# Performance work log

Hardware: AMD Instinct MI355X
Metric: run time of the kernel (lower is better)

The kernel has to match this reference:

```python
import jax, jax.numpy as jnp
import numpy as np

B = 8; C = 256; NH = 8; CH = C // NH; MLP_H = 4 * C; EPS = 1e-5
SIZES = [(56, 56), (28, 28), (14, 14), (7, 7)]  # scales 2..5; scale1 (112x112) passes through


def _layernorm(x, g, b):
    mu = jnp.mean(x, -1, keepdims=True)
    var = jnp.mean((x - mu) ** 2, -1, keepdims=True)
    return (x - mu) * jax.lax.rsqrt(var + EPS) * g + b


def _dwconv(x, w, b, pad):
    # x: [B, C, H, W], w: [C, 1, k, k] depthwise
    out = jax.lax.conv_general_dilated(
        x, w, (1, 1), [(pad, pad), (pad, pad)],
        feature_group_count=x.shape[1],
        dimension_numbers=('NCHW', 'OIHW', 'NCHW'))
    return out + b[None, :, None, None]


def _cpe(x, w, b, size):
    # ConvPosEnc: depthwise 3x3 conv residual on image tokens, cls untouched
    Hh, Ww = size
    Bb, N, Cc = x.shape
    cls_tok, img = x[:, :1], x[:, 1:]
    feat = img.transpose(0, 2, 1).reshape(Bb, Cc, Hh, Ww)
    feat = _dwconv(feat, w, b, 1) + feat
    img = feat.reshape(Bb, Cc, Hh * Ww).transpose(0, 2, 1)
    return jnp.concatenate([cls_tok, img], axis=1)


def _crpe(q, v, ws, bs, size):
    # ConvRelPosEnc: window->head split {3:2, 5:3, 7:3}; EV_hat = q * dwconv(v)
    Hh, Ww = size
    Bb, h, N, Ch = q.shape
    q_img, v_img = q[:, :, 1:], v[:, :, 1:]
    v_map = v_img.transpose(0, 1, 3, 2).reshape(Bb, h * Ch, Hh, Ww)
    splits = [2 * Ch, 3 * Ch, 3 * Ch]
    start = 0; outs = []
    for i, win in enumerate((3, 5, 7)):
        part = v_map[:, start:start + splits[i]]
        outs.append(_dwconv(part, ws[i], bs[i], win // 2))
        start += splits[i]
    conv_v = jnp.concatenate(outs, 1).reshape(Bb, h, Ch, Hh * Ww).transpose(0, 1, 3, 2)
    ev = q_img * conv_v  # [B, h, HW, Ch]
    return jnp.pad(ev, ((0, 0), (0, 0), (1, 0), (0, 0)))  # zero row for cls token


def _factor_att(x, qkv_w, proj_w, proj_b, crpe_ws, crpe_bs, size):
    Bb, N, Cc = x.shape
    qkv = (x @ qkv_w.T).reshape(Bb, N, 3, NH, CH).transpose(2, 0, 3, 1, 4)
    q, k, v = qkv[0], qkv[1], qkv[2]
    k_sm = jax.nn.softmax(k, axis=2)                       # softmax over tokens
    kv = jnp.einsum('bhnk,bhnv->bhkv', k_sm, v)            # [B,h,Ch,Ch]
    fa = jnp.einsum('bhnk,bhkv->bhnv', q, kv)              # [B,h,N,Ch]
    cr = _crpe(q, v, crpe_ws, crpe_bs, size)
    out = (CH ** -0.5 * fa + cr).transpose(0, 2, 1, 3).reshape(Bb, N, Cc)
    return out @ proj_w.T + proj_b


def _interp(x, out_size, size):
    # bilinear (align_corners=False) on image tokens; cls token passes through
    Bb, N, Cc = x.shape
    Hh, Ww = size
    cls_tok, img = x[:, :1], x[:, 1:]
    feat = img.transpose(0, 2, 1).reshape(Bb, Cc, Hh, Ww)
    feat = jax.image.resize(feat, (Bb, Cc, out_size[0], out_size[1]),
                            method='bilinear', antialias=False)
    img = feat.reshape(Bb, Cc, -1).transpose(0, 2, 1)
    return jnp.concatenate([cls_tok, img], axis=1)


def _mlp(x, w1, b1, w2, b2):
    h = jax.nn.gelu(x @ w1.T + b1, approximate=False)
    return h @ w2.T + b2


def _forward(x1, x2, x3, x4, x5, cpe_w, cpe_b, n1_g, n1_b, qkv_w, proj_w, proj_b,
             crpe_w3, crpe_b3, crpe_w5, crpe_b5, crpe_w7, crpe_b7,
             n2_g, n2_b, fc1_w, fc1_b, fc2_w, fc2_b):
    xs = [x2, x3, x4, x5]
    curs = []
    for i in range(4):  # fixed set of 4 scales (not a data-dim loop)
        xi = _cpe(xs[i], cpe_w[i], cpe_b[i], SIZES[i])
        cur = _layernorm(xi, n1_g[i], n1_b[i])
        cur = _factor_att(cur, qkv_w[i], proj_w[i], proj_b[i],
                          (crpe_w3[i], crpe_w5[i], crpe_w7[i]),
                          (crpe_b3[i], crpe_b5[i], crpe_b7[i]), SIZES[i])
        xs[i] = xi
        curs.append(cur)
    c2, c3, c4, c5 = curs
    s2, s3, s4, s5 = SIZES
    # only the interpolations actually used in the residual sums (source has dead ones)
    c2n = c2 + _interp(c3, s2, s3) + _interp(c4, s2, s4)
    c3n = c3 + _interp(c4, s3, s4) + _interp(c2, s3, s2)
    c4n = c4 + _interp(c5, s4, s5) + _interp(c2, s4, s2)
    c5n = c5 + _interp(c4, s5, s4) + _interp(c2, s5, s2)
    curs = [c2n, c3n, c4n, c5n]
    for i in range(4):
        xs[i] = xs[i] + curs[i]
        cur = _layernorm(xs[i], n2_g[i], n2_b[i])
        cur = _mlp(cur, fc1_w, fc1_b, fc2_w, fc2_b)  # MLP shared across scales
        xs[i] = xs[i] + cur
    return (x1, xs[0], xs[1], xs[2], xs[3])


def setup_inputs() -> dict:
    key = jax.random.key(0)
    ks = iter(jax.random.split(key, 40))
    def nrm(shape, scale=1.0):
        return jax.random.normal(next(ks), shape, jnp.float32) * scale
    W = 0.02
    inp = {}
    inp['x1'] = nrm((B, 1 + 112 * 112, C))
    for j, (h, w) in enumerate(SIZES):
        inp['x%d' % (j + 2)] = nrm((B, 1 + h * w, C))
    inp['cpe_w'] = nrm((4, C, 1, 3, 3), W); inp['cpe_b'] = jnp.zeros((4, C))
    inp['n1_g'] = jnp.ones((4, C)); inp['n1_b'] = jnp.zeros((4, C))
    inp['qkv_w'] = nrm((4, 3 * C, C), W)
    inp['proj_w'] = nrm((4, C, C), W); inp['proj_b'] = jnp.zeros((4, C))
    inp['crpe_w3'] = nrm((4, 2 * CH, 1, 3, 3), W); inp['crpe_b3'] = jnp.zeros((4, 2 * CH))
    inp['crpe_w5'] = nrm((4, 3 * CH, 1, 5, 5), W); inp['crpe_b5'] = jnp.zeros((4, 3 * CH))
    inp['crpe_w7'] = nrm((4, 3 * CH, 1, 7, 7), W); inp['crpe_b7'] = jnp.zeros((4, 3 * CH))
    inp['n2_g'] = jnp.ones((4, C)); inp['n2_b'] = jnp.zeros((4, C))
    inp['fc1_w'] = nrm((MLP_H, C), W); inp['fc1_b'] = jnp.zeros((MLP_H,))
    inp['fc2_w'] = nrm((C, MLP_H), W); inp['fc2_b'] = jnp.zeros((C,))
    return inp


def reference(x1, x2, x3, x4, x5, cpe_w, cpe_b, n1_g, n1_b, qkv_w, proj_w, proj_b,
              crpe_w3, crpe_b3, crpe_w5, crpe_b5, crpe_w7, crpe_b7,
              n2_g, n2_b, fc1_w, fc1_b, fc2_w, fc2_b):
    return _forward(x1, x2, x3, x4, x5, cpe_w, cpe_b, n1_g, n1_b, qkv_w, proj_w, proj_b,
                    crpe_w3, crpe_b3, crpe_w5, crpe_b5, crpe_w7, crpe_b7,
                    n2_g, n2_b, fc1_w, fc1_b, fc2_w, fc2_b)
```

## Files before the change

kernel.cpp:

```cpp
#include <hip/hip_runtime.h>
#include <math.h>

typedef unsigned short u16;
typedef __attribute__((ext_vector_type(8))) short bf16x8;
typedef __attribute__((ext_vector_type(4))) float f32x4;

static const int HS[4]     = {56, 28, 14, 7};
static const int NS[4]     = {3137, 785, 197, 50};
static const int ROWOFF[4] = {0, 25096, 31376, 32952};
static const size_t OUTOFF0 = 25692160ull;
#define RTOT 33352

#define DEV __device__ __forceinline__
#define AS1 __attribute__((address_space(1)))
#define AS3 __attribute__((address_space(3)))

DEV u16 f2bf(float x) {
  union { float f; unsigned u; } v; v.f = x;
  unsigned r = v.u + 0x7fffu + ((v.u >> 16) & 1u);
  return (u16)(r >> 16);
}
DEV float bf2f(u16 x) {
  union { unsigned u; float f; } v; v.u = ((unsigned)x) << 16;
  return v.f;
}

struct alignas(8) u16x4s { u16 x, y, z, w; };
struct alignas(16) U16x8 { u16 d[8]; };

DEV int selNS(int s)  { return s == 0 ? 3137 : s == 1 ? 785 : s == 2 ? 197 : 50; }
DEV int selHS(int s)  { return s == 0 ? 56 : s == 1 ? 28 : s == 2 ? 14 : 7; }
DEV int selROW(int s) { return s == 0 ? 0 : s == 1 ? 25096 : s == 2 ? 31376 : 32952; }
DEV int selNPS(int s) { return s == 0 ? 3200 : s == 1 ? 832 : s == 2 ? 256 : 64; }
DEV size_t selKPB(int s) { return s == 0 ? 0ull : s == 1 ? 6553600ull : s == 2 ? 8257536ull : 8781824ull; }
DEV size_t selVPB(int s) { return s == 0 ? 0ull : s == 1 ? 7340032ull : s == 2 ? 11010048ull : 12845056ull; }
DEV int selNC(int s)  { return s == 0 ? 32 : s == 1 ? 8 : s == 2 ? 2 : 1; }
DEV int selNCB(int s) { return s == 0 ? 0 : s == 1 ? 2048 : s == 2 ? 2560 : 2688; }
DEV int row2scale(int row) { return (row >= 25096) + (row >= 31376) + (row >= 32952); }

__global__ void cvt_bf16(const float* __restrict__ src, u16* __restrict__ dst, int n) {
  for (int i = blockIdx.x * blockDim.x + threadIdx.x; i < n; i += gridDim.x * blockDim.x)
    dst[i] = f2bf(src[i]);
}

__global__ void tpw_cpe(const float* __restrict__ src, float* __restrict__ dst) {
  int i = blockIdx.y;
  int e = blockIdx.x * 256 + threadIdx.x;
  if (e < 2304) {
    int c = e / 9, k = e % 9;
    dst[i * 2304 + k * 256 + c] = src[i * 2304 + c * 9 + k];
  }
}

__global__ void copy_f4(const float4* __restrict__ src, float4* __restrict__ dst, int n4) {
  for (int i = blockIdx.x * blockDim.x + threadIdx.x; i < n4; i += gridDim.x * blockDim.x)
    dst[i] = src[i];
}

__global__ void cpe_all(const float* __restrict__ x2, const float* __restrict__ x3,
                        const float* __restrict__ x4, const float* __restrict__ x5,
                        const float* __restrict__ WT, const float* __restrict__ bias,
                        float* __restrict__ out, int total4) {
  for (int idx = blockIdx.x * blockDim.x + threadIdx.x; idx < total4; idx += gridDim.x * blockDim.x) {
    int c4 = (idx & 63) << 2;
    int grow = idx >> 6;
    int s = row2scale(grow);
    int lrow = grow - selROW(s);
    int N = selNS(s), H = selHS(s);
    const float* x = s == 0 ? x2 : s == 1 ? x3 : s == 2 ? x4 : x5;
    int n = lrow % N;
    int b = lrow / N;
    float4 xv = *(const float4*)(x + (size_t)lrow * 256 + c4);
    float4 o = xv;
    if (n > 0) {
      int p = n - 1, h0 = p / H, w0 = p % H;
      float4 acc = *(const float4*)(bias + s * 256 + c4);
      const float* wT = WT + s * 2304;
      #pragma unroll
      for (int kh = 0; kh < 3; ++kh) {
        int hh = h0 + kh - 1;
        if (hh < 0 || hh >= H) continue;
        #pragma unroll
        for (int kw = 0; kw < 3; ++kw) {
          int ww = w0 + kw - 1;
          if (ww < 0 || ww >= H) continue;
          float4 t = *(const float4*)(x + (((size_t)b * N) + 1 + hh * H + ww) * 256 + c4);
          float4 wv = *(const float4*)(wT + (kh * 3 + kw) * 256 + c4);
          acc.x += t.x * wv.x; acc.y += t.y * wv.y;
          acc.z += t.z * wv.z; acc.w += t.w * wv.w;
        }
      }
      o.x += acc.x; o.y += acc.y; o.z += acc.z; o.w += acc.w;
    }
    *(float4*)(out + (size_t)grow * 256 + c4) = o;
  }
}

__global__ void ln_all(const float* __restrict__ x, const float* __restrict__ g,
                       const float* __restrict__ bt, u16* __restrict__ out, int rows) {
  int wid = threadIdx.x >> 6, lane = threadIdx.x & 63;
  int row = blockIdx.x * 4 + wid;
  if (row >= rows) return;
  int s = row2scale(row);
  const float* xr = x + (size_t)row * 256;
  float4 v = *(const float4*)(xr + lane * 4);
  float sm = v.x + v.y + v.z + v.w;
  #pragma unroll
  for (int off = 32; off; off >>= 1) sm += __shfl_down(sm, off);
  sm = __shfl(sm, 0);
  float mu = sm * (1.0f / 256.0f);
  float dx = v.x - mu, dy = v.y - mu, dz = v.z - mu, dw = v.w - mu;
  float q = dx * dx + dy * dy + dz * dz + dw * dw;
  #pragma unroll
  for (int off = 32; off; off >>= 1) q += __shfl_down(q, off);
  q = __shfl(q, 0);
  float rs = rsqrtf(q * (1.0f / 256.0f) + 1e-5f);
  float4 gg = *(const float4*)(g + s * 256 + lane * 4);
  float4 bb = *(const float4*)(bt + s * 256 + lane * 4);
  u16x4s o;
  o.x = f2bf(dx * rs * gg.x + bb.x);
  o.y = f2bf(dy * rs * gg.y + bb.y);
  o.z = f2bf(dz * rs * gg.z + bb.z);
  o.w = f2bf(dw * rs * gg.w + bb.w);
  *(u16x4s*)(out + (size_t)row * 256 + lane * 4) = o;
}

DEV void stage32(const u16* __restrict__ A, const u16* __restrict__ W,
                 u16* dst, int bm, int bn, int M, int K, int k0) {
  int t = threadIdx.x, wv = t >> 6;
  u16* aD = dst;
  u16* bD = dst + 4096;
  #pragma unroll
  for (int iss = 0; iss < 2; ++iss) {
    int s = iss * 256 + t;
    int row = s >> 2, g = s & 3;
    int gel = ((g ^ (row & 3)) << 3);
    int gr = bm + row; if (gr > M - 1) gr = M - 1;
    __builtin_amdgcn_global_load_lds(
        (const AS1 void*)(A + (size_t)gr * K + k0 + gel),
        (AS3 void*)(aD + (size_t)(iss * 256 + wv * 64) * 8), 16, 0, 0);
    __builtin_amdgcn_global_load_lds(
        (const AS1 void*)(W + (size_t)(bn + row) * K + k0 + gel),
        (AS3 void*)(bD + (size_t)(iss * 256 + wv * 64) * 8), 16, 0, 0);
  }
}

template <bool GELU, bool OUT_BF16>
DEV void gemm_core(const u16* __restrict__ A, const u16* __restrict__ W,
                   const float* __restrict__ bias, const float* __restrict__ res,
                   void* __restrict__ outp, int M, int K, int Nout,
                   int bm, int bn, u16* lds) {
  int t = threadIdx.x, lane = t & 63, wv = t >> 6;
  int wr = wv >> 1, wc = wv & 1;
  f32x4 acc[4][4] = {};

  const int nt = K >> 5;
  stage32(A, W, lds, bm, bn, M, K, 0);

  for (int tt = 0; tt < nt; ++tt) {
    __syncthreads();
    if (tt + 1 < nt) stage32(A, W, lds + ((tt + 1) & 1) * 8192, bm, bn, M, K, (tt + 1) << 5);
    const u16* aS = lds + (tt & 1) * 8192;
    const u16* bS = aS + 4096;
    bf16x8 af[4], bfr[4];
    #pragma unroll
    for (int m = 0; m < 4; ++m) {
      int row = wr * 64 + m * 16 + (lane & 15);
      int sg = (lane >> 4) ^ (row & 3);
      af[m] = *(const bf16x8*)(aS + row * 32 + sg * 8);
    }
    #pragma unroll
    for (int n = 0; n < 4; ++n) {
      int row = wc * 64 + n * 16 + (lane & 15);
      int sg = (lane >> 4) ^ (row & 3);
      bfr[n] = *(const bf16x8*)(bS + row * 32 + sg * 8);
    }
    #pragma unroll
    for (int m = 0; m < 4; ++m)
      #pragma unroll
      for (int n = 0; n < 4; ++n)
        acc[m][n] = __builtin_amdgcn_mfma_f32_16x16x32_bf16(af[m], bfr[n], acc[m][n], 0, 0, 0);
  }

  float* eps = (float*)lds;
  #pragma unroll
  for (int pass = 0; pass < 4; ++pass) {
    __syncthreads();
    if (wr == (pass >> 1)) {
      #pragma unroll
      for (int mh = 0; mh < 2; ++mh) {
        int m = (pass & 1) * 2 + mh;
        #pragma unroll
        for (int n = 0; n < 4; ++n) {
          int col = wc * 64 + n * 16 + (lane & 15);
          #pragma unroll
          for (int rg = 0; rg < 4; ++rg) {
            int lr = mh * 16 + ((lane >> 4) << 2) + rg;
            eps[lr * 136 + (((col >> 2) ^ lr) << 2) + (col & 3)] = acc[m][n][rg];
          }
        }
      }
    }
    __syncthreads();
    int lr = t >> 3, c0 = (t & 7) << 4;
    int gr = bm + pass * 32 + lr;
    if (gr >= M) continue;
    int gc = bn + c0;
    float vv[16];
    #pragma unroll
    for (int j = 0; j < 4; ++j) {
      int col = c0 + j * 4;
      float4 f = *(const float4*)(eps + lr * 136 + (((col >> 2) ^ lr) << 2));
      vv[j * 4 + 0] = f.x; vv[j * 4 + 1] = f.y; vv[j * 4 + 2] = f.z; vv[j * 4 + 3] = f.w;
    }
    if (bias) {
      #pragma unroll
      for (int j = 0; j < 4; ++j) {
        float4 bv = *(const float4*)(bias + gc + j * 4);
        vv[j * 4 + 0] += bv.x; vv[j * 4 + 1] += bv.y; vv[j * 4 + 2] += bv.z; vv[j * 4 + 3] += bv.w;
      }
    }
    if (GELU) {
      #pragma unroll
      for (int e = 0; e < 16; ++e) vv[e] = vv[e] / (1.0f + __expf(-1.702f * vv[e]));
    }
    if (res) {
      const float* rp = res + (size_t)gr * Nout + gc;
      #pragma unroll
      for (int j = 0; j < 4; ++j) {
        float4 rv = *(const float4*)(rp + j * 4);
        vv[j * 4 + 0] += rv.x; vv[j * 4 + 1] += rv.y; vv[j * 4 + 2] += rv.z; vv[j * 4 + 3] += rv.w;
      }
    }
    if (OUT_BF16) {
      u16* op = (u16*)outp + (size_t)gr * Nout + gc;
      U16x8 p0, p1;
      #pragma unroll
      for (int e = 0; e < 8; ++e) { p0.d[e] = f2bf(vv[e]); p1.d[e] = f2bf(vv[8 + e]); }
      *(U16x8*)op = p0;
      *(U16x8*)(op + 8) = p1;
    } else {
      float* op = (float*)outp + (size_t)gr * Nout + gc;
      #pragma unroll
      for (int j = 0; j < 4; ++j)
        *(float4*)(op + j * 4) = make_float4(vv[j * 4], vv[j * 4 + 1], vv[j * 4 + 2], vv[j * 4 + 3]);
    }
  }
}

DEV int xcd_swizzle(int orig, int nblk) {
  int q = nblk >> 3, r = nblk & 7;
  int xcd = orig & 7, lin = orig >> 3;
  return (xcd < r ? xcd * (q + 1) : r * (q + 1) + (xcd - r) * q) + lin;
}

template <bool GELU, bool OUT_BF16>
__launch_bounds__(256, 4)
__global__ void gemm_mfma(const u16* __restrict__ A, const u16* __restrict__ W,
                          const float* __restrict__ bias, const float* __restrict__ res,
                          void* __restrict__ outp, int M, int K, int Nout, int nnt) {
  __shared__ __align__(16) u16 lds[16384];
  int wg = xcd_swizzle(blockIdx.x, gridDim.x);
  int bm = (wg / nnt) << 7, bn = (wg % nnt) << 7;
  gemm_core<GELU, OUT_BF16>(A, W, bias, res, outp, M, K, Nout, bm, bn, lds);
}

struct GrpArgs {
  const u16* A[4];
  const u16* W[4];
  const float* bias[4];
  size_t outoff[4];
  int M[4];
  int pref[5];
};

template <bool OUT_BF16>
__launch_bounds__(256, 4)
__global__ void gemm_grp(GrpArgs ga, void* __restrict__ outbase, int K, int Nout, int nnt) {
  __shared__ __align__(16) u16 lds[16384];
  int wg = xcd_swizzle(blockIdx.x, gridDim.x);
  int i = (wg >= ga.pref[1]) + (wg >= ga.pref[2]) + (wg >= ga.pref[3]);
  int local = wg - ga.pref[i];
  int bm = (local / nnt) << 7, bn = (local % nnt) << 7;
  void* outp = OUT_BF16 ? (void*)((u16*)outbase + ga.outoff[i])
                        : (void*)((float*)outbase + ga.outoff[i]);
  gemm_core<false, OUT_BF16>(ga.A[i], ga.W[i], ga.bias[i], nullptr, outp,
                             ga.M[i], K, Nout, bm, bn, lds);
}

__global__ void tp_all(const u16* __restrict__ T2, u16* __restrict__ KP,
                       u16* __restrict__ VP, u16* __restrict__ VPI) {
  int z = blockIdx.z, s = z >> 3, b = z & 7;
  int N = selNS(s), H = selHS(s);
  int nt0 = blockIdx.x * 64;
  if (nt0 >= N) return;
  int NPs = selNPS(s);
  int hw64 = H * 64;
  const u16* T2i = T2 + (size_t)selROW(s) * 768;
  u16* kpb = KP + selKPB(s);
  u16* vpb = VP + selKPB(s);
  u16* vib = VPI + selVPB(s);
  __shared__ u16 tl[64][66];
  int c0 = blockIdx.y * 64, t = threadIdx.x;
  for (int e = t; e < 4096; e += 256) {
    int n_l = e >> 6, c_l = e & 63;
    int n = nt0 + n_l;
    tl[n_l][c_l] = (n < N) ? T2i[((size_t)b * N + n) * 768 + 256 + c0 + c_l] : (u16)0;
  }
  __syncthreads();
  for (int e = t; e < 4096; e += 256) {
    int c_l = e >> 6, n_l = e & 63;
    int n = nt0 + n_l;
    if (n >= N) continue;
    int cg = c0 + c_l;
    u16 val = tl[n_l][c_l];
    if (cg < 256) {
      kpb[(size_t)(b * 256 + cg) * NPs + n] = val;
    } else {
      int cc = cg - 256;
      vpb[(size_t)(b * 256 + cc) * NPs + n] = val;
      if (n >= 1) {
        int p = n - 1;
        vib[(size_t)(b * 256 + cc) * hw64 + (p / H) * 64 + (p % H)] = val;
      }
    }
  }
}

__global__ void ksm_all(const u16* __restrict__ KP, float* __restrict__ mx,
                        float* __restrict__ se) {
  int s = blockIdx.z, b = blockIdx.y;
  int N = selNS(s), NPs = selNPS(s);
  int wv = threadIdx.x >> 6, lane = threadIdx.x & 63;
  int cg = blockIdx.x * 4 + wv;
  const u16* kp = KP + selKPB(s) + (size_t)(b * 256 + cg) * NPs;
  float m = -1e30f, sm = 0.f;
  for (int n = lane; n < N; n += 64) {
    float v = bf2f(kp[n]);
    float nm = fmaxf(m, v);
    sm = sm * __expf(m - nm) + __expf(v - nm);
    m = nm;
  }
  #pragma unroll
  for (int off = 1; off < 64; off <<= 1) {
    float mo = __shfl_xor(m, off), so = __shfl_xor(sm, off);
    float nm = fmaxf(m, mo);
    sm = sm * __expf(m - nm) + so * __expf(mo - nm);
    m = nm;
  }
  if (lane == 0) { mx[s * 2048 + b * 256 + cg] = m; se[s * 2048 + b * 256 + cg] = sm; }
}

__launch_bounds__(1024)
__global__ void kv_partial_all(const u16* __restrict__ KP, const u16* __restrict__ VP,
                               const float* __restrict__ mx, float* __restrict__ part) {
  __shared__ float kl[32][65];
  __shared__ float vl[32][65];
  int blk = blockIdx.x;
  int s = (blk >= selNCB(1)) + (blk >= selNCB(2)) + (blk >= selNCB(3));
  int local = blk - selNCB(s);
  int NC = selNC(s);
  int chunk = local % NC;
  int bh = local / NC;
  int b = bh >> 3, h = bh & 7;
  int N = selNS(s), NPs = selNPS(s);
  int chunkrows = (N + NC - 1) / NC;
  const u16* kpb = KP + selKPB(s);
  const u16* vpb = VP + selKPB(s);
  int t = threadIdx.x;
  int i = t >> 5, j = t & 31;
  float acc = 0.f;
  int n0s = chunk * chunkrows, n1s = min(N, n0s + chunkrows);
  for (int n0 = n0s; n0 < n1s; n0 += 64) {
    #pragma unroll
    for (int e = t; e < 2048; e += 1024) {
      int c = e >> 6, nn = e & 63;
      int n = n0 + nn;
      bool ok = (n < n1s);
      kl[c][nn] = ok ? bf2f(kpb[(size_t)(b * 256 + h * 32 + c) * NPs + n]) : -1e30f;
      vl[c][nn] = ok ? bf2f(vpb[(size_t)(b * 256 + h * 32 + c) * NPs + n]) : 0.f;
    }
    __syncthreads();
    #pragma unroll
    for (int e = t; e < 2048; e += 1024) {
      int c = e >> 6, nn = e & 63;
      kl[c][nn] = __expf(kl[c][nn] - mx[s * 2048 + b * 256 + h * 32 + c]);
    }
    __syncthreads();
    #pragma unroll
    for (int nn = 0; nn < 64; ++nn) acc += kl[i][nn] * vl[j][nn];
    __syncthreads();
  }
  part[(size_t)blk * 1024 + t] = acc;
}

__global__ void kv_reduce_all(const float* __restrict__ part, const float* __restrict__ se,
                              float* __restrict__ kv) {
  int bh = blockIdx.x, s = blockIdx.y;
  int NC = selNC(s), base = selNCB(s);
  int t = threadIdx.x;
  int i = t >> 5;
  int b = bh >> 3, h = bh & 7;
  float sm = 0.f;
  for (int c = 0; c < NC; ++c) sm += part[(size_t)(base + bh * NC + c) * 1024 + t];
  kv[(size_t)s * 65536 + bh * 1024 + t] = sm / se[s * 2048 + b * 256 + h * 32 + i];
}

template <int KS, int C0>
__global__ void crpe_all(const u16* __restrict__ VPI, const float* __restrict__ w,
                         const float* __restrict__ bias, u16* __restrict__ CVPI, int CS) {
  constexpr int pad = KS / 2;
  int z = blockIdx.z;
  int s = (z >= 2) + (z >= 3) + (z >= 4);
  int sub = z - (s == 0 ? 0 : s + 1);
  int RS = (s == 0) ? 2 : 1;
  int H = selHS(s);
  int c = blockIdx.x, b = blockIdx.y;
  int G = (H + 7) >> 3;
  int hpb = (H + RS - 1) / RS;
  int h0b = sub * hpb;
  int h1b = min(H, h0b + hpb);
  size_t plane = selVPB(s) + (size_t)(b * 256 + C0 + c) * (size_t)(H * 64);
  const u16* vp = VPI + plane;
  u16* op = CVPI + plane;
  float wreg[KS * KS];
  #pragma unroll
  for (int e = 0; e < KS * KS; ++e) wreg[e] = w[(s * CS + c) * KS * KS + e];
  float bb = bias[s * CS + c];
  int ntask = (h1b - h0b) * G;
  for (int task = threadIdx.x; task < ntask; task += 256) {
    int g = task % G;
    int h = h0b + task / G;
    int w0 = g << 3;
    float o[8];
    #pragma unroll
    for (int e = 0; e < 8; ++e) o[e] = bb;
    #pragma unroll
    for (int kh = 0; kh < KS; ++kh) {
      int hh = h + kh - pad;
      if (hh < 0 || hh >= H) continue;
      const u16* rowp = vp + hh * 64;
      U16x8 ch0 = {}, ch1, ch2;
      if (w0 >= 8) ch0 = *(const U16x8*)(rowp + w0 - 8);
      ch1 = *(const U16x8*)(rowp + w0);
      ch2 = *(const U16x8*)(rowp + w0 + 8);
      float tv[24];
      #pragma unroll
      for (int j2 = 8 - pad; j2 <= 15 + pad; ++j2) {
        u16 raw = (j2 < 8) ? ch0.d[j2] : (j2 < 16 ? ch1.d[j2 - 8] : ch2.d[j2 - 16]);
        tv[j2] = bf2f(raw);
      }
      #pragma unroll
      for (int kw = 0; kw < KS; ++kw) {
        float wv = wreg[kh * KS + kw];
        #pragma unroll
        for (int e = 0; e < 8; ++e) o[e] += tv[8 + e + kw - pad] * wv;
      }
    }
    U16x8 pk;
    #pragma unroll
    for (int e = 0; e < 8; ++e) pk.d[e] = f2bf(o[e]);
    *(U16x8*)(op + h * 64 + w0) = pk;
  }
}

__global__ void att_all(const u16* __restrict__ T2, const u16* __restrict__ CVPI,
                        const float* __restrict__ kvg, u16* __restrict__ attp) {
  int s = blockIdx.z, b = blockIdx.y;
  int N = selNS(s), H = selHS(s);
  int n0 = blockIdx.x * 16;
  if (n0 >= N) return;
  __shared__ float kvl[8192];
  __shared__ float ql[256];
  __shared__ float cl[16][260];
  int t = threadIdx.x;
  int hw64 = H * 64;
  const u16* T2i = T2 + (size_t)selROW(s) * 768;
  u16* attpi = attp + (size_t)selROW(s) * 256;
  const u16* cvb = CVPI + selVPB(s);
  for (int e = t; e < 8192; e += 256) kvl[e] = kvg[(size_t)s * 65536 + b * 8192 + e];
  for (int e = t; e < 4096; e += 256) {
    int c = e >> 4, nn = e & 15;
    int n = n0 + nn;
    float v = 0.f;
    if (n >= 1 && n < N) {
      int p = n - 1;
      v = bf2f(cvb[(size_t)(b * 256 + c) * hw64 + (p / H) * 64 + (p % H)]);
    }
    cl[nn][c] = v;
  }
  int h = t >> 5, j = t & 31;
  for (int nn = 0; nn < 16; ++nn) {
    int n = n0 + nn;
    if (n >= N) break;
    __syncthreads();
    ql[t] = bf2f(T2i[((size_t)(b * N + n)) * 768 + t]);
    __syncthreads();
    float fa = 0.f;
    const float* kvh = kvl + h * 1024;
    #pragma unroll
    for (int k = 0; k < 32; ++k) fa += ql[h * 32 + k] * kvh[k * 32 + j];
    float v = 0.17677669529663687f * fa + ql[t] * cl[nn][t];
    attpi[(((size_t)b * N) + n) * 256 + t] = f2bf(v);
  }
}

DEV float4 bsample4(const float* __restrict__ src, int b, int Ns, int Hs,
                    int oh, int ow, int Hi, int c4) {
  float scale = (float)Hs / (float)Hi;
  float sy = (oh + 0.5f) * scale - 0.5f;
  float sx = (ow + 0.5f) * scale - 0.5f;
  float fy0 = floorf(sy), fx0 = floorf(sx);
  float fy = sy - fy0, fx = sx - fx0;
  int y0 = (int)fy0, x0 = (int)fx0;
  int y0c = min(max(y0, 0), Hs - 1), y1c = min(max(y0 + 1, 0), Hs - 1);
  int x0c = min(max(x0, 0), Hs - 1), x1c = min(max(x0 + 1, 0), Hs - 1);
  const float* base = src + ((size_t)b * Ns + 1) * 256 + c4;
  float4 v00 = *(const float4*)(base + (size_t)(y0c * Hs + x0c) * 256);
  float4 v01 = *(const float4*)(base + (size_t)(y0c * Hs + x1c) * 256);
  float4 v10 = *(const float4*)(base + (size_t)(y1c * Hs + x0c) * 256);
  float4 v11 = *(const float4*)(base + (size_t)(y1c * Hs + x1c) * 256);
  float w00 = (1.f - fy) * (1.f - fx), w01 = (1.f - fy) * fx;
  float w10 = fy * (1.f - fx), w11 = fy * fx;
  float4 r;
  r.x = w00 * v00.x + w01 * v01.x + w10 * v10.x + w11 * v11.x;
  r.y = w00 * v00.y + w01 * v01.y + w10 * v10.y + w11 * v11.y;
  r.z = w00 * v00.z + w01 * v01.z + w10 * v10.z + w11 * v11.z;
  r.w = w00 * v00.w + w01 * v01.w + w10 * v10.w + w11 * v11.w;
  return r;
}

__global__ void combine_all(float* __restrict__ xi, const float* __restrict__ cc, int total4) {
  for (int idx = blockIdx.x * blockDim.x + threadIdx.x; idx < total4; idx += gridDim.x * blockDim.x) {
    int c4 = (idx & 63) << 2;
    int grow = idx >> 6;
    int s = row2scale(grow);
    int lrow = grow - selROW(s);
    int Ni = selNS(s), Hi = selHS(s);
    int sa = s == 0 ? 1 : s == 1 ? 2 : s == 2 ? 3 : 2;
    int sb = s == 0 ? 2 : 0;
    const float* srcA = cc + (size_t)selROW(sa) * 256;
    const float* srcB = cc + (size_t)selROW(sb) * 256;
    int HsA = selHS(sa), NsA = selNS(sa);
    int HsB = selHS(sb), NsB = selNS(sb);
    int n = lrow % Ni;
    int b = lrow / Ni;
    float4 add = *(const float4*)(cc + (size_t)grow * 256 + c4);
    if (n == 0) {
      float4 a = *(const float4*)(srcA + ((size_t)b * NsA) * 256 + c4);
      float4 bb = *(const float4*)(srcB + ((size_t)b * NsB) * 256 + c4);
      add.x += a.x + bb.x; add.y += a.y + bb.y;
      add.z += a.z + bb.z; add.w += a.w + bb.w;
    } else {
      int p = n - 1, oh = p / Hi, ow = p % Hi;
      float4 a = bsample4(srcA, b, NsA, HsA, oh, ow, Hi, c4);
      float4 bb = bsample4(srcB, b, NsB, HsB, oh, ow, Hi, c4);
      add.x += a.x + bb.x; add.y += a.y + bb.y;
      add.z += a.z + bb.z; add.w += a.w + bb.w;
    }
    float* xp = xi + (size_t)grow * 256 + c4;
    float4 cur = *(const float4*)xp;
    cur.x += add.x; cur.y += add.y; cur.z += add.z; cur.w += add.w;
    *(float4*)xp = cur;
  }
}

extern "C" void kernel_launch(void* const* d_in, const int* in_sizes, int n_in,
                              void* d_out, int out_size, void* d_ws, size_t ws_size,
                              hipStream_t stream) {
  const float* x1 = (const float*)d_in[0];
  const float* x2 = (const float*)d_in[1];
  const float* x3 = (const float*)d_in[2];
  const float* x4 = (const float*)d_in[3];
  const float* x5 = (const float*)d_in[4];
  const float* cpe_w  = (const float*)d_in[5];
  const float* cpe_b  = (const float*)d_in[6];
  const float* n1_g   = (const float*)d_in[7];
  const float* n1_b   = (const float*)d_in[8];
  const float* qkv_w  = (const float*)d_in[9];
  const float* proj_w = (const float*)d_in[10];
  const float* proj_b = (const float*)d_in[11];
  const float* crpe_w3 = (const float*)d_in[12];
  const float* crpe_b3 = (const float*)d_in[13];
  const float* crpe_w5 = (const float*)d_in[14];
  const float* crpe_b5 = (const float*)d_in[15];
  const float* crpe_w7 = (const float*)d_in[16];
  const float* crpe_b7 = (const float*)d_in[17];
  const float* n2_g   = (const float*)d_in[18];
  const float* n2_b   = (const float*)d_in[19];
  const float* fc1_w  = (const float*)d_in[20];
  const float* fc1_b  = (const float*)d_in[21];
  const float* fc2_w  = (const float*)d_in[22];
  const float* fc2_b  = (const float*)d_in[23];

  float* ws = (float*)d_ws;
  float* XI   = ws;
  float* CC   = XI + 8538112;
  u16*   T1   = (u16*)(CC + 8538112);
  u16*   T2   = T1 + 8538112;
  u16*   KP   = T2 + 34152448;
  u16*   VP   = KP + 8912896;
  u16*   VPI  = VP + 8912896;
  u16*   CVPI = VPI + 13762560;
  float* PRT  = (float*)CVPI;
  float* MX   = (float*)(CVPI + 13762560);
  float* SE   = MX + 8192;
  float* KV   = SE + 8192;
  u16*   WQ   = (u16*)(KV + 262144);
  u16*   WP   = WQ + 786432;
  u16*   W1   = WP + 262144;
  u16*   W2   = W1 + 262144;
  float* WT   = (float*)(W2 + 262144);

  float* out = (float*)d_out;

  cvt_bf16<<<1536, 256, 0, stream>>>(qkv_w, WQ, 786432);
  cvt_bf16<<<512, 256, 0, stream>>>(proj_w, WP, 262144);
  cvt_bf16<<<512, 256, 0, stream>>>(fc1_w, W1, 262144);
  cvt_bf16<<<512, 256, 0, stream>>>(fc2_w, W2, 262144);
  tpw_cpe<<<dim3(9, 4), 256, 0, stream>>>(cpe_w, WT);

  copy_f4<<<8192, 256, 0, stream>>>((const float4*)x1, (float4*)out, 25692160 / 4);

  int nmt[4], prefQ[5], prefP[5];
  prefQ[0] = prefP[0] = 0;
  for (int i = 0; i < 4; ++i) {
    nmt[i] = (8 * NS[i] + 127) / 128;
    prefQ[i + 1] = prefQ[i] + nmt[i] * 6;
    prefP[i + 1] = prefP[i] + nmt[i] * 2;
  }

  cpe_all<<<8192, 256, 0, stream>>>(x2, x3, x4, x5, WT, cpe_b, XI, RTOT * 64);
  ln_all<<<(RTOT + 3) / 4, 256, 0, stream>>>(XI, n1_g, n1_b, T1, RTOT);

  {
    GrpArgs ga;
    for (int i = 0; i < 4; ++i) {
      ga.A[i] = T1 + (size_t)ROWOFF[i] * 256;
      ga.W[i] = WQ + (size_t)i * 196608;
      ga.bias[i] = nullptr;
      ga.outoff[i] = (size_t)ROWOFF[i] * 768;
      ga.M[i] = 8 * NS[i];
    }
    for (int e = 0; e < 5; ++e) ga.pref[e] = prefQ[e];
    gemm_grp<true><<<prefQ[4], 256, 0, stream>>>(ga, T2, 256, 768, 6);
  }

  hipMemsetAsync(VPI, 0, 13762560ull * 2, stream);
  tp_all<<<dim3(50, 8, 32), 256, 0, stream>>>(T2, KP, VP, VPI);
  ksm_all<<<dim3(64, 8, 4), 256, 0, stream>>>(KP, MX, SE);
  kv_partial_all<<<2752, 1024, 0, stream>>>(KP, VP, MX, PRT);
  kv_reduce_all<<<dim3(64, 4), 1024, 0, stream>>>(PRT, SE, KV);
  crpe_all<3, 0><<<dim3(64, 8, 5), 256, 0, stream>>>(VPI, crpe_w3, crpe_b3, CVPI, 64);
  crpe_all<5, 64><<<dim3(96, 8, 5), 256, 0, stream>>>(VPI, crpe_w5, crpe_b5, CVPI, 96);
  crpe_all<7, 160><<<dim3(96, 8, 5), 256, 0, stream>>>(VPI, crpe_w7, crpe_b7, CVPI, 96);
  att_all<<<dim3(197, 8, 4), 256, 0, stream>>>(T2, CVPI, KV, T1);

  {
    GrpArgs ga;
    for (int i = 0; i < 4; ++i) {
      ga.A[i] = T1 + (size_t)ROWOFF[i] * 256;
      ga.W[i] = WP + (size_t)i * 65536;
      ga.bias[i] = proj_b + i * 256;
      ga.outoff[i] = (size_t)ROWOFF[i] * 256;
      ga.M[i] = 8 * NS[i];
    }
    for (int e = 0; e < 5; ++e) ga.pref[e] = prefP[e];
    gemm_grp<false><<<prefP[4], 256, 0, stream>>>(ga, CC, 256, 256, 2);
  }

  combine_all<<<8192, 256, 0, stream>>>(XI, CC, RTOT * 64);

  ln_all<<<(RTOT + 3) / 4, 256, 0, stream>>>(XI, n2_g, n2_b, T1, RTOT);
  int nmtT = (RTOT + 127) / 128;
  gemm_mfma<true, true><<<nmtT * 8, 256, 0, stream>>>(T1, W1, fc1_b, nullptr, (void*)T2,
                                                      RTOT, 256, 1024, 8);
  gemm_mfma<false, false><<<nmtT * 2, 256, 0, stream>>>(T2, W2, fc2_b, XI, out + OUTOFF0,
                                                        RTOT, 1024, 256, 2);
}
```

Before: 520.4 us.

## Pad per-scale token rows and fuse QKV transpose, CPE+LN, combine+LN into GEMMs

Switches activations to a padded per-scale row layout (tile-aligned per batch) so GEMM tiles never straddle scales and need no row clamping. The QKV GEMM epilogue writes Q, the transposed K/V planes and the spatial V image directly, which removes the separate transpose kernel and the wide QKV buffer. CPE is fused with the first LayerNorm and the residual combine with the second, and fc2 gets a dedicated kernel with a scattered residual/output epilogue. In exchange, padding rows add some wasted GEMM work, and the epilogues become more complex, with scattered stores.

```diff
diff --git a/kernel.cpp b/kernel.cpp
--- a/kernel.cpp
+++ b/kernel.cpp
@@ -5,11 +5,8 @@
 typedef __attribute__((ext_vector_type(8))) short bf16x8;
 typedef __attribute__((ext_vector_type(4))) float f32x4;
 
-static const int HS[4]     = {56, 28, 14, 7};
-static const int NS[4]     = {3137, 785, 197, 50};
-static const int ROWOFF[4] = {0, 25096, 31376, 32952};
-static const size_t OUTOFF0 = 25692160ull;
-#define RTOT 33352
+#define MP 36864
+#define OUTOFF0 25692160ull
 
 #define DEV __device__ __forceinline__
 #define AS1 __attribute__((address_space(1)))
@@ -28,15 +25,31 @@
 struct alignas(8) u16x4s { u16 x, y, z, w; };
 struct alignas(16) U16x8 { u16 d[8]; };
 
-DEV int selNS(int s)  { return s == 0 ? 3137 : s == 1 ? 785 : s == 2 ? 197 : 50; }
-DEV int selHS(int s)  { return s == 0 ? 56 : s == 1 ? 28 : s == 2 ? 14 : 7; }
-DEV int selROW(int s) { return s == 0 ? 0 : s == 1 ? 25096 : s == 2 ? 31376 : 32952; }
-DEV int selNPS(int s) { return s == 0 ? 3200 : s == 1 ? 832 : s == 2 ? 256 : 64; }
-DEV size_t selKPB(int s) { return s == 0 ? 0ull : s == 1 ? 6553600ull : s == 2 ? 8257536ull : 8781824ull; }
-DEV size_t selVPB(int s) { return s == 0 ? 0ull : s == 1 ? 7340032ull : s == 2 ? 11010048ull : 12845056ull; }
-DEV int selNC(int s)  { return s == 0 ? 32 : s == 1 ? 8 : s == 2 ? 2 : 1; }
-DEV int selNCB(int s) { return s == 0 ? 0 : s == 1 ? 2048 : s == 2 ? 2560 : 2688; }
-DEV int row2scale(int row) { return (row >= 25096) + (row >= 31376) + (row >= 32952); }
+DEV int rs_s(int row)   { return (row >= 25600) + (row >= 33792) + (row >= 35840); }
+DEV int selPB(int s)    { return s == 0 ? 0 : s == 1 ? 25600 : s == 2 ? 33792 : 35840; }
+DEV int selNPAD(int s)  { return s == 0 ? 3200 : s == 1 ? 1024 : s == 2 ? 256 : 128; }
+DEV int selN(int s)     { return s == 0 ? 3137 : s == 1 ? 785 : s == 2 ? 197 : 50; }
+DEV int selH(int s)     { return s == 0 ? 56 : s == 1 ? 28 : s == 2 ? 14 : 7; }
+DEV int selRO(int s)    { return s == 0 ? 0 : s == 1 ? 25096 : s == 2 ? 31376 : 32952; }
+DEV size_t selKPB(int s){ return s == 0 ? 0ull : s == 1 ? 6553600ull : s == 2 ? 8650752ull : 9175040ull; }
+DEV size_t selVPB(int s){ return s == 0 ? 0ull : s == 1 ? 7340032ull : s == 2 ? 11010048ull : 12845056ull; }
+DEV int selNC(int s)    { return s == 0 ? 32 : s == 1 ? 8 : s == 2 ? 2 : 1; }
+DEV int selNCB(int s)   { return s == 0 ? 0 : s == 1 ? 2048 : s == 2 ? 2560 : 2688; }
+DEV unsigned selHM(int s){ return s == 0 ? 74899u : s == 1 ? 149797u : s == 2 ? 299594u : 599187u; }
+
+DEV void sbn(int row, int s, int& b, int& n) {
+  int l = row - selPB(s);
+  if (s == 0)      { b = l / 3200; n = l - b * 3200; }
+  else if (s == 1) { b = l >> 10; n = l & 1023; }
+  else if (s == 2) { b = l >> 8;  n = l & 255; }
+  else             { b = l >> 7;  n = l & 127; }
+}
+
+DEV int xcd_swizzle(int orig, int nblk) {
+  int q = nblk >> 3, r = nblk & 7;
+  int xcd = orig & 7, lin = orig >> 3;
+  return (xcd < r ? xcd * (q + 1) : r * (q + 1) + (xcd - r) * q) + lin;
+}
 
 __global__ void cvt_bf16(const float* __restrict__ src, u16* __restrict__ dst, int n) {
   for (int i = blockIdx.x * blockDim.x + threadIdx.x; i < n; i += gridDim.x * blockDim.x)
@@ -57,24 +70,25 @@
     dst[i] = src[i];
 }
 
-__global__ void cpe_all(const float* __restrict__ x2, const float* __restrict__ x3,
-                        const float* __restrict__ x4, const float* __restrict__ x5,
-                        const float* __restrict__ WT, const float* __restrict__ bias,
-                        float* __restrict__ out, int total4) {
-  for (int idx = blockIdx.x * blockDim.x + threadIdx.x; idx < total4; idx += gridDim.x * blockDim.x) {
-    int c4 = (idx & 63) << 2;
-    int grow = idx >> 6;
-    int s = row2scale(grow);
-    int lrow = grow - selROW(s);
-    int N = selNS(s), H = selHS(s);
+__global__ void cpe_ln_all(const float* __restrict__ x2, const float* __restrict__ x3,
+                           const float* __restrict__ x4, const float* __restrict__ x5,
+                           const float* __restrict__ WT, const float* __restrict__ cpe_b,
+                           const float* __restrict__ n1g, const float* __restrict__ n1b,
+                           float* __restrict__ XI, u16* __restrict__ T1) {
+  int wid = threadIdx.x >> 6, lane = threadIdx.x & 63;
+  int row = blockIdx.x * 4 + wid;
+  if (row >= MP) return;
+  int s = rs_s(row);
+  int b, n; sbn(row, s, b, n);
+  int N = selN(s), H = selH(s);
+  int c4 = lane * 4;
+  float4 v = make_float4(0.f, 0.f, 0.f, 0.f);
+  if (n < N) {
     const float* x = s == 0 ? x2 : s == 1 ? x3 : s == 2 ? x4 : x5;
-    int n = lrow % N;
-    int b = lrow / N;
-    float4 xv = *(const float4*)(x + (size_t)lrow * 256 + c4);
-    float4 o = xv;
+    v = *(const float4*)(x + ((size_t)b * N + n) * 256 + c4);
     if (n > 0) {
       int p = n - 1, h0 = p / H, w0 = p % H;
-      float4 acc = *(const float4*)(bias + s * 256 + c4);
+      float4 acc = *(const float4*)(cpe_b + s * 256 + c4);
       const float* wT = WT + s * 2304;
       #pragma unroll
       for (int kh = 0; kh < 3; ++kh) {
@@ -84,26 +98,16 @@
         for (int kw = 0; kw < 3; ++kw) {
           int ww = w0 + kw - 1;
           if (ww < 0 || ww >= H) continue;
-          float4 t = *(const float4*)(x + (((size_t)b * N) + 1 + hh * H + ww) * 256 + c4);
+          float4 t = *(const float4*)(x + ((size_t)b * N + 1 + hh * H + ww) * 256 + c4);
           float4 wv = *(const float4*)(wT + (kh * 3 + kw) * 256 + c4);
           acc.x += t.x * wv.x; acc.y += t.y * wv.y;
           acc.z += t.z * wv.z; acc.w += t.w * wv.w;
         }
       }
-      o.x += acc.x; o.y += acc.y; o.z += acc.z; o.w += acc.w;
-    }
-    *(float4*)(out + (size_t)grow * 256 + c4) = o;
-  }
-}
-
-__global__ void ln_all(const float* __restrict__ x, const float* __restrict__ g,
-                       const float* __restrict__ bt, u16* __restrict__ out, int rows) {
-  int wid = threadIdx.x >> 6, lane = threadIdx.x & 63;
-  int row = blockIdx.x * 4 + wid;
-  if (row >= rows) return;
-  int s = row2scale(row);
-  const float* xr = x + (size_t)row * 256;
-  float4 v = *(const float4*)(xr + lane * 4);
+      v.x += acc.x; v.y += acc.y; v.z += acc.z; v.w += acc.w;
+    }
+  }
+  *(float4*)(XI + (size_t)row * 256 + c4) = v;
   float sm = v.x + v.y + v.z + v.w;
   #pragma unroll
   for (int off = 32; off; off >>= 1) sm += __shfl_down(sm, off);
@@ -115,29 +119,28 @@
   for (int off = 32; off; off >>= 1) q += __shfl_down(q, off);
   q = __shfl(q, 0);
   float rs = rsqrtf(q * (1.0f / 256.0f) + 1e-5f);
-  float4 gg = *(const float4*)(g + s * 256 + lane * 4);
-  float4 bb = *(const float4*)(bt + s * 256 + lane * 4);
+  float4 gg = *(const float4*)(n1g + s * 256 + c4);
+  float4 bb = *(const float4*)(n1b + s * 256 + c4);
   u16x4s o;
   o.x = f2bf(dx * rs * gg.x + bb.x);
   o.y = f2bf(dy * rs * gg.y + bb.y);
   o.z = f2bf(dz * rs * gg.z + bb.z);
   o.w = f2bf(dw * rs * gg.w + bb.w);
-  *(u16x4s*)(out + (size_t)row * 256 + lane * 4) = o;
+  *(u16x4s*)(T1 + (size_t)row * 256 + c4) = o;
 }
 
 DEV void stage32(const u16* __restrict__ A, const u16* __restrict__ W,
-                 u16* dst, int bm, int bn, int M, int K, int k0) {
+                 u16* dst, int bm, int bn, int K, int k0) {
   int t = threadIdx.x, wv = t >> 6;
   u16* aD = dst;
   u16* bD = dst + 4096;
   #pragma unroll
   for (int iss = 0; iss < 2; ++iss) {
-    int s = iss * 256 + t;
-    int row = s >> 2, g = s & 3;
+    int sI = iss * 256 + t;
+    int row = sI >> 2, g = sI & 3;
     int gel = ((g ^ (row & 3)) << 3);
-    int gr = bm + row; if (gr > M - 1) gr = M - 1;
     __builtin_amdgcn_global_load_lds(
-        (const AS1 void*)(A + (size_t)gr * K + k0 + gel),
+        (const AS1 void*)(A + (size_t)(bm + row) * K + k0 + gel),
         (AS3 void*)(aD + (size_t)(iss * 256 + wv * 64) * 8), 16, 0, 0);
     __builtin_amdgcn_global_load_lds(
         (const AS1 void*)(W + (size_t)(bn + row) * K + k0 + gel),
@@ -145,21 +148,15 @@
   }
 }
 
-template <bool GELU, bool OUT_BF16>
-DEV void gemm_core(const u16* __restrict__ A, const u16* __restrict__ W,
-                   const float* __restrict__ bias, const float* __restrict__ res,
-                   void* __restrict__ outp, int M, int K, int Nout,
-                   int bm, int bn, u16* lds) {
+DEV void mainloop(const u16* __restrict__ A, const u16* __restrict__ W, int K,
+                  int bm, int bn, u16* lds, f32x4 (&acc)[4][4]) {
   int t = threadIdx.x, lane = t & 63, wv = t >> 6;
   int wr = wv >> 1, wc = wv & 1;
-  f32x4 acc[4][4] = {};
-
   const int nt = K >> 5;
-  stage32(A, W, lds, bm, bn, M, K, 0);
-
+  stage32(A, W, lds, bm, bn, K, 0);
   for (int tt = 0; tt < nt; ++tt) {
     __syncthreads();
-    if (tt + 1 < nt) stage32(A, W, lds + ((tt + 1) & 1) * 8192, bm, bn, M, K, (tt + 1) << 5);
+    if (tt + 1 < nt) stage32(A, W, lds + ((tt + 1) & 1) * 8192, bm, bn, K, (tt + 1) << 5);
     const u16* aS = lds + (tt & 1) * 8192;
     const u16* bS = aS + 4096;
     bf16x8 af[4], bfr[4];
@@ -181,148 +178,182 @@
       for (int n = 0; n < 4; ++n)
         acc[m][n] = __builtin_amdgcn_mfma_f32_16x16x32_bf16(af[m], bfr[n], acc[m][n], 0, 0, 0);
   }
-
+}
+
+DEV void epi_dump(const f32x4 (&acc)[4][4], int pass, float* eps) {
+  int t = threadIdx.x, lane = t & 63, wv = t >> 6;
+  int wr = wv >> 1, wc = wv & 1;
+  if (wr != (pass >> 1)) return;
+  #pragma unroll
+  for (int mh = 0; mh < 2; ++mh) {
+    int m = (pass & 1) * 2 + mh;
+    #pragma unroll
+    for (int n = 0; n < 4; ++n) {
+      int col = wc * 64 + n * 16 + (lane & 15);
+      #pragma unroll
+      for (int rg = 0; rg < 4; ++rg)
+        eps[(mh * 16 + ((lane >> 4) << 2) + rg) * 132 + col] = acc[m][n][rg];
+    }
+  }
+}
+
+template <bool GELU, bool BF16>
+DEV void epi_rowmajor(const float* eps, int pass, void* outp, const float* bias,
+                      int bm, int bn, int Nout) {
+  int t = threadIdx.x;
+  int lr = t >> 3, cb = (t & 7) * 4;
+  int gr = bm + pass * 32 + lr;
+  #pragma unroll
+  for (int j = 0; j < 4; ++j) {
+    int col = cb + j * 32;
+    float4 f = *(const float4*)(eps + lr * 132 + col);
+    int gc = bn + col;
+    if (bias) {
+      float4 bv = *(const float4*)(bias + gc);
+      f.x += bv.x; f.y += bv.y; f.z += bv.z; f.w += bv.w;
+    }
+    if (GELU) {
+      f.x /= (1.0f + __expf(-1.702f * f.x));
+      f.y /= (1.0f + __expf(-1.702f * f.y));
+      f.z /= (1.0f + __expf(-1.702f * f.z));
+      f.w /= (1.0f + __expf(-1.702f * f.w));
+    }
+    if (BF16) {
+      u16x4s p;
+      p.x = f2bf(f.x); p.y = f2bf(f.y); p.z = f2bf(f.z); p.w = f2bf(f.w);
+      *(u16x4s*)((u16*)outp + (size_t)gr * Nout + gc) = p;
+    } else {
+      *(float4*)((float*)outp + (size_t)gr * Nout + gc) = f;
+    }
+  }
+}
+
+template <bool GELU, bool BF16>
+__launch_bounds__(256, 4)
+__global__ void gemm_std(const u16* __restrict__ A, const u16* __restrict__ W,
+                         const float* __restrict__ bias, void* __restrict__ outp,
+                         int K, int Nout, int nnt) {
+  __shared__ __align__(16) u16 lds[16384];
+  int wg = xcd_swizzle(blockIdx.x, gridDim.x);
+  int bm = (wg / nnt) << 7, bn = (wg % nnt) << 7;
+  f32x4 acc[4][4] = {};
+  mainloop(A, W, K, bm, bn, lds, acc);
   float* eps = (float*)lds;
   #pragma unroll
   for (int pass = 0; pass < 4; ++pass) {
     __syncthreads();
-    if (wr == (pass >> 1)) {
+    epi_dump(acc, pass, eps);
+    __syncthreads();
+    epi_rowmajor<GELU, BF16>(eps, pass, outp, bias, bm, bn, Nout);
+  }
+}
+
+__launch_bounds__(256, 4)
+__global__ void qkv_gemm(const u16* __restrict__ A, const u16* __restrict__ WQ,
+                         u16* __restrict__ Q16, u16* __restrict__ KP,
+                         u16* __restrict__ VP, u16* __restrict__ VPI) {
+  __shared__ __align__(16) u16 lds[16384];
+  int wg = xcd_swizzle(blockIdx.x, gridDim.x);
+  int mt = wg / 6, ct = wg % 6;
+  int bm = mt << 7, bn = ct << 7;
+  int s = rs_s(bm);
+  f32x4 acc[4][4] = {};
+  mainloop(A, WQ + (size_t)s * 196608, 256, bm, bn, lds, acc);
+  float* eps = (float*)lds;
+  int b, nb; sbn(bm, s, b, nb);
+  int NPAD = selNPAD(s), H = selH(s), HW = H * H;
+  unsigned hmag = selHM(s);
+  #pragma unroll
+  for (int pass = 0; pass < 4; ++pass) {
+    __syncthreads();
+    epi_dump(acc, pass, eps);
+    __syncthreads();
+    if (ct < 2) {
+      epi_rowmajor<false, true>(eps, pass, Q16, nullptr, bm, bn, 256);
+    } else {
+      int t = threadIdx.x;
+      int c = t >> 1, half = t & 1;
+      bool isK = (ct < 4);
+      int cg = bn - (isK ? 256 : 512) + c;
+      int n0 = nb + pass * 32 + half * 16;
+      float vals[16];
       #pragma unroll
-      for (int mh = 0; mh < 2; ++mh) {
-        int m = (pass & 1) * 2 + mh;
+      for (int r = 0; r < 16; ++r) vals[r] = eps[(half * 16 + r) * 132 + c];
+      U16x8 p0, p1;
+      #pragma unroll
+      for (int e = 0; e < 8; ++e) { p0.d[e] = f2bf(vals[e]); p1.d[e] = f2bf(vals[8 + e]); }
+      u16* pbase = (isK ? KP : VP) + selKPB(s) + (size_t)(b * 256 + cg) * NPAD + n0;
+      *(U16x8*)pbase = p0;
+      *(U16x8*)(pbase + 8) = p1;
+      if (!isK) {
+        u16* vplane = VPI + selVPB(s) + (size_t)(b * 256 + cg) * (H * 64);
         #pragma unroll
-        for (int n = 0; n < 4; ++n) {
-          int col = wc * 64 + n * 16 + (lane & 15);
-          #pragma unroll
-          for (int rg = 0; rg < 4; ++rg) {
-            int lr = mh * 16 + ((lane >> 4) << 2) + rg;
-            eps[lr * 136 + (((col >> 2) ^ lr) << 2) + (col & 3)] = acc[m][n][rg];
+        for (int r = 0; r < 16; ++r) {
+          int n = n0 + r;
+          if (n >= 1 && n <= HW) {
+            int p = n - 1;
+            int qd = (int)(((unsigned)p * hmag) >> 22);
+            vplane[qd * 64 + (p - qd * H)] = f2bf(vals[r]);
           }
         }
       }
     }
-    __syncthreads();
-    int lr = t >> 3, c0 = (t & 7) << 4;
-    int gr = bm + pass * 32 + lr;
-    if (gr >= M) continue;
-    int gc = bn + c0;
-    float vv[16];
-    #pragma unroll
-    for (int j = 0; j < 4; ++j) {
-      int col = c0 + j * 4;
-      float4 f = *(const float4*)(eps + lr * 136 + (((col >> 2) ^ lr) << 2));
-      vv[j * 4 + 0] = f.x; vv[j * 4 + 1] = f.y; vv[j * 4 + 2] = f.z; vv[j * 4 + 3] = f.w;
-    }
-    if (bias) {
-      #pragma unroll
-      for (int j = 0; j < 4; ++j) {
-        float4 bv = *(const float4*)(bias + gc + j * 4);
-        vv[j * 4 + 0] += bv.x; vv[j * 4 + 1] += bv.y; vv[j * 4 + 2] += bv.z; vv[j * 4 + 3] += bv.w;
-      }
-    }
-    if (GELU) {
-      #pragma unroll
-      for (int e = 0; e < 16; ++e) vv[e] = vv[e] / (1.0f + __expf(-1.702f * vv[e]));
-    }
-    if (res) {
-      const float* rp = res + (size_t)gr * Nout + gc;
-      #pragma unroll
-      for (int j = 0; j < 4; ++j) {
-        float4 rv = *(const float4*)(rp + j * 4);
-        vv[j * 4 + 0] += rv.x; vv[j * 4 + 1] += rv.y; vv[j * 4 + 2] += rv.z; vv[j * 4 + 3] += rv.w;
-      }
-    }
-    if (OUT_BF16) {
-      u16* op = (u16*)outp + (size_t)gr * Nout + gc;
-      U16x8 p0, p1;
-      #pragma unroll
-      for (int e = 0; e < 8; ++e) { p0.d[e] = f2bf(vv[e]); p1.d[e] = f2bf(vv[8 + e]); }
-      *(U16x8*)op = p0;
-      *(U16x8*)(op + 8) = p1;
-    } else {
-      float* op = (float*)outp + (size_t)gr * Nout + gc;
-      #pragma unroll
-      for (int j = 0; j < 4; ++j)
-        *(float4*)(op + j * 4) = make_float4(vv[j * 4], vv[j * 4 + 1], vv[j * 4 + 2], vv[j * 4 + 3]);
-    }
-  }
-}
-
-DEV int xcd_swizzle(int orig, int nblk) {
-  int q = nblk >> 3, r = nblk & 7;
-  int xcd = orig & 7, lin = orig >> 3;
-  return (xcd < r ? xcd * (q + 1) : r * (q + 1) + (xcd - r) * q) + lin;
-}
-
-template <bool GELU, bool OUT_BF16>
+  }
+}
+
 __launch_bounds__(256, 4)
-__global__ void gemm_mfma(const u16* __restrict__ A, const u16* __restrict__ W,
-                          const float* __restrict__ bias, const float* __restrict__ res,
-                          void* __restrict__ outp, int M, int K, int Nout, int nnt) {
+__global__ void proj_gemm(const u16* __restrict__ A, const u16* __restrict__ WP,
+                          const float* __restrict__ proj_b, float* __restrict__ CC) {
   __shared__ __align__(16) u16 lds[16384];
   int wg = xcd_swizzle(blockIdx.x, gridDim.x);
-  int bm = (wg / nnt) << 7, bn = (wg % nnt) << 7;
-  gemm_core<GELU, OUT_BF16>(A, W, bias, res, outp, M, K, Nout, bm, bn, lds);
-}
-
-struct GrpArgs {
-  const u16* A[4];
-  const u16* W[4];
-  const float* bias[4];
-  size_t outoff[4];
-  int M[4];
-  int pref[5];
-};
-
-template <bool OUT_BF16>
+  int bm = (wg >> 1) << 7, bn = (wg & 1) << 7;
+  int s = rs_s(bm);
+  f32x4 acc[4][4] = {};
+  mainloop(A, WP + (size_t)s * 65536, 256, bm, bn, lds, acc);
+  float* eps = (float*)lds;
+  #pragma unroll
+  for (int pass = 0; pass < 4; ++pass) {
+    __syncthreads();
+    epi_dump(acc, pass, eps);
+    __syncthreads();
+    epi_rowmajor<false, false>(eps, pass, CC, proj_b + s * 256, bm, bn, 256);
+  }
+}
+
 __launch_bounds__(256, 4)
-__global__ void gemm_grp(GrpArgs ga, void* __restrict__ outbase, int K, int Nout, int nnt) {
+__global__ void fc2_gemm(const u16* __restrict__ A, const u16* __restrict__ W2,
+                         const float* __restrict__ fc2_b, const float* __restrict__ XI,
+                         float* __restrict__ out) {
   __shared__ __align__(16) u16 lds[16384];
   int wg = xcd_swizzle(blockIdx.x, gridDim.x);
-  int i = (wg >= ga.pref[1]) + (wg >= ga.pref[2]) + (wg >= ga.pref[3]);
-  int local = wg - ga.pref[i];
-  int bm = (local / nnt) << 7, bn = (local % nnt) << 7;
-  void* outp = OUT_BF16 ? (void*)((u16*)outbase + ga.outoff[i])
-                        : (void*)((float*)outbase + ga.outoff[i]);
-  gemm_core<false, OUT_BF16>(ga.A[i], ga.W[i], ga.bias[i], nullptr, outp,
-                             ga.M[i], K, Nout, bm, bn, lds);
-}
-
-__global__ void tp_all(const u16* __restrict__ T2, u16* __restrict__ KP,
-                       u16* __restrict__ VP, u16* __restrict__ VPI) {
-  int z = blockIdx.z, s = z >> 3, b = z & 7;
-  int N = selNS(s), H = selHS(s);
-  int nt0 = blockIdx.x * 64;
-  if (nt0 >= N) return;
-  int NPs = selNPS(s);
-  int hw64 = H * 64;
-  const u16* T2i = T2 + (size_t)selROW(s) * 768;
-  u16* kpb = KP + selKPB(s);
-  u16* vpb = VP + selKPB(s);
-  u16* vib = VPI + selVPB(s);
-  __shared__ u16 tl[64][66];
-  int c0 = blockIdx.y * 64, t = threadIdx.x;
-  for (int e = t; e < 4096; e += 256) {
-    int n_l = e >> 6, c_l = e & 63;
-    int n = nt0 + n_l;
-    tl[n_l][c_l] = (n < N) ? T2i[((size_t)b * N + n) * 768 + 256 + c0 + c_l] : (u16)0;
-  }
-  __syncthreads();
-  for (int e = t; e < 4096; e += 256) {
-    int c_l = e >> 6, n_l = e & 63;
-    int n = nt0 + n_l;
+  int bm = (wg >> 1) << 7, bn = (wg & 1) << 7;
+  f32x4 acc[4][4] = {};
+  mainloop(A, W2, 1024, bm, bn, lds, acc);
+  float* eps = (float*)lds;
+  int s = rs_s(bm);
+  int b, nb; sbn(bm, s, b, nb);
+  int N = selN(s), RO = selRO(s);
+  #pragma unroll
+  for (int pass = 0; pass < 4; ++pass) {
+    __syncthreads();
+    epi_dump(acc, pass, eps);
+    __syncthreads();
+    int t = threadIdx.x;
+    int lr = t >> 3, cb = (t & 7) * 4;
+    int n = nb + pass * 32 + lr;
     if (n >= N) continue;
-    int cg = c0 + c_l;
-    u16 val = tl[n_l][c_l];
-    if (cg < 256) {
-      kpb[(size_t)(b * 256 + cg) * NPs + n] = val;
-    } else {
-      int cc = cg - 256;
-      vpb[(size_t)(b * 256 + cc) * NPs + n] = val;
-      if (n >= 1) {
-        int p = n - 1;
-        vib[(size_t)(b * 256 + cc) * hw64 + (p / H) * 64 + (p % H)] = val;
-      }
+    int prow = bm + pass * 32 + lr;
+    size_t orow = (size_t)RO + (size_t)b * N + n;
+    #pragma unroll
+    for (int j = 0; j < 4; ++j) {
+      int col = cb + j * 32;
+      float4 f = *(const float4*)(eps + lr * 132 + col);
+      int gc = bn + col;
+      float4 bv = *(const float4*)(fc2_b + gc);
+      float4 rv = *(const float4*)(XI + (size_t)prow * 256 + gc);
+      f.x += bv.x + rv.x; f.y += bv.y + rv.y;
+      f.z += bv.z + rv.z; f.w += bv.w + rv.w;
+      *(float4*)(out + OUTOFF0 + orow * 256 + gc) = f;
     }
   }
 }
@@ -330,10 +361,10 @@
 __global__ void ksm_all(const u16* __restrict__ KP, float* __restrict__ mx,
                         float* __restrict__ se) {
   int s = blockIdx.z, b = blockIdx.y;
-  int N = selNS(s), NPs = selNPS(s);
+  int N = selN(s), NPAD = selNPAD(s);
   int wv = threadIdx.x >> 6, lane = threadIdx.x & 63;
   int cg = blockIdx.x * 4 + wv;
-  const u16* kp = KP + selKPB(s) + (size_t)(b * 256 + cg) * NPs;
+  const u16* kp = KP + selKPB(s) + (size_t)(b * 256 + cg) * NPAD;
   float m = -1e30f, sm = 0.f;
   for (int n = lane; n < N; n += 64) {
     float v = bf2f(kp[n]);
@@ -363,7 +394,7 @@
   int chunk = local % NC;
   int bh = local / NC;
   int b = bh >> 3, h = bh & 7;
-  int N = selNS(s), NPs = selNPS(s);
+  int N = selN(s), NPAD = selNPAD(s);
   int chunkrows = (N + NC - 1) / NC;
   const u16* kpb = KP + selKPB(s);
   const u16* vpb = VP + selKPB(s);
@@ -377,8 +408,8 @@
       int c = e >> 6, nn = e & 63;
       int n = n0 + nn;
       bool ok = (n < n1s);
-      kl[c][nn] = ok ? bf2f(kpb[(size_t)(b * 256 + h * 32 + c) * NPs + n]) : -1e30f;
-      vl[c][nn] = ok ? bf2f(vpb[(size_t)(b * 256 + h * 32 + c) * NPs + n]) : 0.f;
+      kl[c][nn] = ok ? bf2f(kpb[(size_t)(b * 256 + h * 32 + c) * NPAD + n]) : -1e30f;
+      vl[c][nn] = ok ? bf2f(vpb[(size_t)(b * 256 + h * 32 + c) * NPAD + n]) : 0.f;
     }
     __syncthreads();
     #pragma unroll
@@ -414,7 +445,7 @@
   int s = (z >= 2) + (z >= 3) + (z >= 4);
   int sub = z - (s == 0 ? 0 : s + 1);
   int RS = (s == 0) ? 2 : 1;
-  int H = selHS(s);
+  int H = selH(s);
   int c = blockIdx.x, b = blockIdx.y;
   int G = (H + 7) >> 3;
   int hpb = (H + RS - 1) / RS;
@@ -464,10 +495,10 @@
   }
 }
 
-__global__ void att_all(const u16* __restrict__ T2, const u16* __restrict__ CVPI,
+__global__ void att_all(const u16* __restrict__ Q16, const u16* __restrict__ CVPI,
                         const float* __restrict__ kvg, u16* __restrict__ attp) {
   int s = blockIdx.z, b = blockIdx.y;
-  int N = selNS(s), H = selHS(s);
+  int N = selN(s), H = selH(s);
   int n0 = blockIdx.x * 16;
   if (n0 >= N) return;
   __shared__ float kvl[8192];
@@ -475,8 +506,7 @@
   __shared__ float cl[16][260];
   int t = threadIdx.x;
   int hw64 = H * 64;
-  const u16* T2i = T2 + (size_t)selROW(s) * 768;
-  u16* attpi = attp + (size_t)selROW(s) * 256;
+  size_t rowbase = (size_t)selPB(s) + (size_t)b * selNPAD(s);
   const u16* cvb = CVPI + selVPB(s);
   for (int e = t; e < 8192; e += 256) kvl[e] = kvg[(size_t)s * 65536 + b * 8192 + e];
   for (int e = t; e < 4096; e += 256) {
@@ -494,19 +524,18 @@
     int n = n0 + nn;
     if (n >= N) break;
     __syncthreads();
-    ql[t] = bf2f(T2i[((size_t)(b * N + n)) * 768 + t]);
+    ql[t] = bf2f(Q16[(rowbase + n) * 256 + t]);
     __syncthreads();
     float fa = 0.f;
     const float* kvh = kvl + h * 1024;
     #pragma unroll
     for (int k = 0; k < 32; ++k) fa += ql[h * 32 + k] * kvh[k * 32 + j];
     float v = 0.17677669529663687f * fa + ql[t] * cl[nn][t];
-    attpi[(((size_t)b * N) + n) * 256 + t] = f2bf(v);
-  }
-}
-
-DEV float4 bsample4(const float* __restrict__ src, int b, int Ns, int Hs,
-                    int oh, int ow, int Hi, int c4) {
+    attp[(rowbase + n) * 256 + t] = f2bf(v);
+  }
+}
+
+DEV float4 bs4(const float* __restrict__ base, int Hs, int oh, int ow, int Hi, int c4) {
   float scale = (float)Hs / (float)Hi;
   float sy = (oh + 0.5f) * scale - 0.5f;
   float sx = (ow + 0.5f) * scale - 0.5f;
@@ -515,11 +544,11 @@
   int y0 = (int)fy0, x0 = (int)fx0;
   int y0c = min(max(y0, 0), Hs - 1), y1c = min(max(y0 + 1, 0), Hs - 1);
   int x0c = min(max(x0, 0), Hs - 1), x1c = min(max(x0 + 1, 0), Hs - 1);
-  const float* base = src + ((size_t)b * Ns + 1) * 256 + c4;
-  float4 v00 = *(const float4*)(base + (size_t)(y0c * Hs + x0c) * 256);
-  float4 v01 = *(const float4*)(base + (size_t)(y0c * Hs + x1c) * 256);
-  float4 v10 = *(const float4*)(base + (size_t)(y1c * Hs + x0c) * 256);
-  float4 v11 = *(const float4*)(base + (size_t)(y1c * Hs + x1c) * 256);
+  const float* ib = base + 256 + c4;
+  float4 v00 = *(const float4*)(ib + (size_t)(y0c * Hs + x0c) * 256);
+  float4 v01 = *(const float4*)(ib + (size_t)(y0c * Hs + x1c) * 256);
+  float4 v10 = *(const float4*)(ib + (size_t)(y1c * Hs + x0c) * 256);
+  float4 v11 = *(const float4*)(ib + (size_t)(y1c * Hs + x1c) * 256);
   float w00 = (1.f - fy) * (1.f - fx), w01 = (1.f - fy) * fx;
   float w10 = fy * (1.f - fx), w11 = fy * fx;
   float4 r;
@@ -530,39 +559,61 @@
   return r;
 }
 
-__global__ void combine_all(float* __restrict__ xi, const float* __restrict__ cc, int total4) {
-  for (int idx = blockIdx.x * blockDim.x + threadIdx.x; idx < total4; idx += gridDim.x * blockDim.x) {
-    int c4 = (idx & 63) << 2;
-    int grow = idx >> 6;
-    int s = row2scale(grow);
-    int lrow = grow - selROW(s);
-    int Ni = selNS(s), Hi = selHS(s);
+__global__ void combine_ln_all(float* __restrict__ XI, const float* __restrict__ CC,
+                               const float* __restrict__ n2g, const float* __restrict__ n2b,
+                               u16* __restrict__ T1) {
+  int wid = threadIdx.x >> 6, lane = threadIdx.x & 63;
+  int row = blockIdx.x * 4 + wid;
+  if (row >= MP) return;
+  int s = rs_s(row);
+  int b, n; sbn(row, s, b, n);
+  int N = selN(s), Hi = selH(s);
+  int c4 = lane * 4;
+  float4 v;
+  if (n < N) {
+    float4 add = *(const float4*)(CC + (size_t)row * 256 + c4);
     int sa = s == 0 ? 1 : s == 1 ? 2 : s == 2 ? 3 : 2;
-    int sb = s == 0 ? 2 : 0;
-    const float* srcA = cc + (size_t)selROW(sa) * 256;
-    const float* srcB = cc + (size_t)selROW(sb) * 256;
-    int HsA = selHS(sa), NsA = selNS(sa);
-    int HsB = selHS(sb), NsB = selNS(sb);
-    int n = lrow % Ni;
-    int b = lrow / Ni;
-    float4 add = *(const float4*)(cc + (size_t)grow * 256 + c4);
+    int sb_ = s == 0 ? 2 : 0;
+    const float* baseA = CC + ((size_t)selPB(sa) + (size_t)b * selNPAD(sa)) * 256;
+    const float* baseB = CC + ((size_t)selPB(sb_) + (size_t)b * selNPAD(sb_)) * 256;
     if (n == 0) {
-      float4 a = *(const float4*)(srcA + ((size_t)b * NsA) * 256 + c4);
-      float4 bb = *(const float4*)(srcB + ((size_t)b * NsB) * 256 + c4);
-      add.x += a.x + bb.x; add.y += a.y + bb.y;
-      add.z += a.z + bb.z; add.w += a.w + bb.w;
+      float4 a = *(const float4*)(baseA + c4);
+      float4 bb2 = *(const float4*)(baseB + c4);
+      add.x += a.x + bb2.x; add.y += a.y + bb2.y;
+      add.z += a.z + bb2.z; add.w += a.w + bb2.w;
     } else {
       int p = n - 1, oh = p / Hi, ow = p % Hi;
-      float4 a = bsample4(srcA, b, NsA, HsA, oh, ow, Hi, c4);
-      float4 bb = bsample4(srcB, b, NsB, HsB, oh, ow, Hi, c4);
-      add.x += a.x + bb.x; add.y += a.y + bb.y;
-      add.z += a.z + bb.z; add.w += a.w + bb.w;
-    }
-    float* xp = xi + (size_t)grow * 256 + c4;
-    float4 cur = *(const float4*)xp;
-    cur.x += add.x; cur.y += add.y; cur.z += add.z; cur.w += add.w;
-    *(float4*)xp = cur;
-  }
+      float4 a = bs4(baseA, selH(sa), oh, ow, Hi, c4);
+      float4 bb2 = bs4(baseB, selH(sb_), oh, ow, Hi, c4);
+      add.x += a.x + bb2.x; add.y += a.y + bb2.y;
+      add.z += a.z + bb2.z; add.w += a.w + bb2.w;
+    }
+    float* xp = XI + (size_t)row * 256 + c4;
+    v = *(const float4*)xp;
+    v.x += add.x; v.y += add.y; v.z += add.z; v.w += add.w;
+    *(float4*)xp = v;
+  } else {
+    v = make_float4(0.f, 0.f, 0.f, 0.f);
+  }
+  float sm = v.x + v.y + v.z + v.w;
+  #pragma unroll
+  for (int off = 32; off; off >>= 1) sm += __shfl_down(sm, off);
+  sm = __shfl(sm, 0);
+  float mu = sm * (1.0f / 256.0f);
+  float dx = v.x - mu, dy = v.y - mu, dz = v.z - mu, dw = v.w - mu;
+  float q = dx * dx + dy * dy + dz * dz + dw * dw;
+  #pragma unroll
+  for (int off = 32; off; off >>= 1) q += __shfl_down(q, off);
+  q = __shfl(q, 0);
+  float rs = rsqrtf(q * (1.0f / 256.0f) + 1e-5f);
+  float4 gg = *(const float4*)(n2g + s * 256 + c4);
+  float4 bb = *(const float4*)(n2b + s * 256 + c4);
+  u16x4s o;
+  o.x = f2bf(dx * rs * gg.x + bb.x);
+  o.y = f2bf(dy * rs * gg.y + bb.y);
+  o.z = f2bf(dz * rs * gg.z + bb.z);
+  o.w = f2bf(dw * rs * gg.w + bb.w);
+  *(u16x4s*)(T1 + (size_t)row * 256 + c4) = o;
 }
 
 extern "C" void kernel_launch(void* const* d_in, const int* in_sizes, int n_in,
@@ -595,14 +646,16 @@
 
   float* ws = (float*)d_ws;
   float* XI   = ws;
-  float* CC   = XI + 8538112;
-  u16*   T1   = (u16*)(CC + 8538112);
-  u16*   T2   = T1 + 8538112;
-  u16*   KP   = T2 + 34152448;
-  u16*   VP   = KP + 8912896;
-  u16*   VPI  = VP + 8912896;
+  float* CC   = XI + 9437184;
+  u16*   T1   = (u16*)(CC + 9437184);
+  float* REG  = (float*)(T1 + 9437184);
+  u16*   Q16  = (u16*)REG;
+  u16*   KP   = Q16 + 9437184;
+  u16*   VP   = KP + 9437184;
+  u16*   VPI  = VP + 9437184;
   u16*   CVPI = VPI + 13762560;
   float* PRT  = (float*)CVPI;
+  u16*   T2   = (u16*)REG;
   float* MX   = (float*)(CVPI + 13762560);
   float* SE   = MX + 8192;
   float* KV   = SE + 8192;
@@ -614,6 +667,7 @@
 
   float* out = (float*)d_out;
 
+  hipMemsetAsync(VPI, 0, 13762560ull * 2, stream);
   cvt_bf16<<<1536, 256, 0, stream>>>(qkv_w, WQ, 786432);
   cvt_bf16<<<512, 256, 0, stream>>>(proj_w, WP, 262144);
   cvt_bf16<<<512, 256, 0, stream>>>(fc1_w, W1, 262144);
@@ -622,59 +676,22 @@
 
   copy_f4<<<8192, 256, 0, stream>>>((const float4*)x1, (float4*)out, 25692160 / 4);
 
-  int nmt[4], prefQ[5], prefP[5];
-  prefQ[0] = prefP[0] = 0;
-  for (int i = 0; i < 4; ++i) {
-    nmt[i] = (8 * NS[i] + 127) / 128;
-    prefQ[i + 1] = prefQ[i] + nmt[i] * 6;
-    prefP[i + 1] = prefP[i] + nmt[i] * 2;
-  }
-
-  cpe_all<<<8192, 256, 0, stream>>>(x2, x3, x4, x5, WT, cpe_b, XI, RTOT * 64);
-  ln_all<<<(RTOT + 3) / 4, 256, 0, stream>>>(XI, n1_g, n1_b, T1, RTOT);
-
-  {
-    GrpArgs ga;
-    for (int i = 0; i < 4; ++i) {
-      ga.A[i] = T1 + (size_t)ROWOFF[i] * 256;
-      ga.W[i] = WQ + (size_t)i * 196608;
-      ga.bias[i] = nullptr;
-      ga.outoff[i] = (size_t)ROWOFF[i] * 768;
-      ga.M[i] = 8 * NS[i];
-    }
-    for (int e = 0; e < 5; ++e) ga.pref[e] = prefQ[e];
-    gemm_grp<true><<<prefQ[4], 256, 0, stream>>>(ga, T2, 256, 768, 6);
-  }
-
-  hipMemsetAsync(VPI, 0, 13762560ull * 2, stream);
-  tp_all<<<dim3(50, 8, 32), 256, 0, stream>>>(T2, KP, VP, VPI);
+  cpe_ln_all<<<MP / 4, 256, 0, stream>>>(x2, x3, x4, x5, WT, cpe_b, n1_g, n1_b, XI, T1);
+
+  qkv_gemm<<<288 * 6, 256, 0, stream>>>(T1, WQ, Q16, KP, VP, VPI);
+
   ksm_all<<<dim3(64, 8, 4), 256, 0, stream>>>(KP, MX, SE);
   kv_partial_all<<<2752, 1024, 0, stream>>>(KP, VP, MX, PRT);
   kv_reduce_all<<<dim3(64, 4), 1024, 0, stream>>>(PRT, SE, KV);
   crpe_all<3, 0><<<dim3(64, 8, 5), 256, 0, stream>>>(VPI, crpe_w3, crpe_b3, CVPI, 64);
   crpe_all<5, 64><<<dim3(96, 8, 5), 256, 0, stream>>>(VPI, crpe_w5, crpe_b5, CVPI, 96);
   crpe_all<7, 160><<<dim3(96, 8, 5), 256, 0, stream>>>(VPI, crpe_w7, crpe_b7, CVPI, 96);
-  att_all<<<dim3(197, 8, 4), 256, 0, stream>>>(T2, CVPI, KV, T1);
-
-  {
-    GrpArgs ga;
-    for (int i = 0; i < 4; ++i) {
-      ga.A[i] = T1 + (size_t)ROWOFF[i] * 256;
-      ga.W[i] = WP + (size_t)i * 65536;
-      ga.bias[i] = proj_b + i * 256;
-      ga.outoff[i] = (size_t)ROWOFF[i] * 256;
-      ga.M[i] = 8 * NS[i];
-    }
-    for (int e = 0; e < 5; ++e) ga.pref[e] = prefP[e];
-    gemm_grp<false><<<prefP[4], 256, 0, stream>>>(ga, CC, 256, 256, 2);
-  }
-
-  combine_all<<<8192, 256, 0, stream>>>(XI, CC, RTOT * 64);
-
-  ln_all<<<(RTOT + 3) / 4, 256, 0, stream>>>(XI, n2_g, n2_b, T1, RTOT);
-  int nmtT = (RTOT + 127) / 128;
-  gemm_mfma<true, true><<<nmtT * 8, 256, 0, stream>>>(T1, W1, fc1_b, nullptr, (void*)T2,
-                                                      RTOT, 256, 1024, 8);
-  gemm_mfma<false, false><<<nmtT * 2, 256, 0, stream>>>(T2, W2, fc2_b, XI, out + OUTOFF0,
-                                                        RTOT, 1024, 256, 2);
-}
+  att_all<<<dim3(197, 8, 4), 256, 0, stream>>>(Q16, CVPI, KV, T1);
+
+  proj_gemm<<<288 * 2, 256, 0, stream>>>(T1, WP, proj_b, CC);
+
+  combine_ln_all<<<MP / 4, 256, 0, stream>>>(XI, CC, n2_g, n2_b, T1);
+
+  gemm_std<true, true><<<288 * 8, 256, 0, stream>>>(T1, W1, fc1_b, (void*)T2, 256, 1024, 8);
+  fc2_gemm<<<288 * 2, 256, 0, stream>>>(T2, W2, fc2_b, XI, out);
+}
```

Result: faster. 489.3 us (-6.0%).
